# Kernel tuning notes

Measured on AMD Instinct MI355X. Metric: run time of the kernel, lower is better.

Reference implementation:

```python
import jax, jax.numpy as jnp
import numpy as np

N_NODES = 50000
N_EDGES = 800000
D_IN = 96
HID = 128


def _glorot(key, shape):
    fan_in, fan_out = shape[0], shape[1]
    lim = np.sqrt(6.0 / (fan_in + fan_out)).astype(np.float32)
    return jax.random.uniform(key, shape, jnp.float32, -lim, lim)


def setup_inputs() -> dict:
    key = jax.random.key(0)
    ks = jax.random.split(key, 12)
    x = jax.random.normal(ks[0], (N_NODES, D_IN), jnp.float32)
    edge_index = jax.random.randint(ks[1], (2, N_EDGES), 0, N_NODES)
    return {
        "x": x,
        "edge_index": edge_index,
        "W_in": _glorot(ks[2], (D_IN, HID)),
        "b_in": jnp.zeros((HID,), jnp.float32),
        "W1": _glorot(ks[3], (HID, HID)),
        "b1": jnp.zeros((HID,), jnp.float32),
        "W2": _glorot(ks[4], (HID, HID)),
        "b2": jnp.zeros((HID,), jnp.float32),
        "Wm1": _glorot(ks[5], (2 * HID, HID)),
        "bm1": jnp.zeros((HID,), jnp.float32),
        "Wm2": _glorot(ks[6], (HID, 1)),
        "bm2": jnp.zeros((1,), jnp.float32),
    }


def _gcn_conv(h, W, b, src, dst, n_nodes):
    # PyG GCNConv with add_self_loops=True, normalize=True:
    # out = D^{-1/2} (A + I) D^{-1/2} (h W) + b, aggregating x_j (source) into dst.
    loop = jnp.arange(n_nodes)
    row = jnp.concatenate([src, loop])  # source / j
    col = jnp.concatenate([dst, loop])  # target / i
    deg = jax.ops.segment_sum(jnp.ones(row.shape, h.dtype), col, num_segments=n_nodes)
    dinv = jnp.where(deg > 0, jax.lax.rsqrt(deg), 0.0)
    norm = dinv[row] * dinv[col]  # [E+N]
    xw = h @ W  # [N, H]
    msg = xw[row] * norm[:, None]  # gather + scale, [E+N, H]
    out = jax.ops.segment_sum(msg, col, num_segments=n_nodes)  # scatter-add
    return out + b


def reference(x, edge_index, W_in, b_in, W1, b1, W2, b2, Wm1, bm1, Wm2, bm2):
    src, dst = edge_index[0], edge_index[1]
    n = x.shape[0]
    h = jax.nn.relu(x @ W_in + b_in)  # dropout is identity at inference
    h = jax.nn.relu(_gcn_conv(h, W1, b1, src, dst, n))
    h = jax.nn.relu(_gcn_conv(h, W2, b2, src, dst, n))
    ef = jnp.concatenate([h[src], h[dst]], axis=1)  # [E, 2H]
    hid = jax.nn.relu(ef @ Wm1 + bm1)
    logits = (hid @ Wm2 + bm2)[:, 0]  # [E]
    return logits
```

## Files before the change

### kernel.cpp

```cpp
#include <hip/hip_runtime.h>

#define N_NODES 50000
#define N_EDGES 800000
#define D_IN 96
#define HID 128
#define NB 391
#define BCAP 3072
#define AECAP 1408

typedef __attribute__((ext_vector_type(8))) _Float16 halfx8;
typedef __attribute__((ext_vector_type(4))) _Float16 half4v;
typedef __attribute__((ext_vector_type(2))) _Float16 half2v;
typedef __attribute__((ext_vector_type(16))) float f32x16;
typedef __attribute__((ext_vector_type(8))) float f32x8;

__device__ inline float dot2acc(half2v a, half2v b, float c) {
#if __has_builtin(__builtin_amdgcn_fdot2)
    return __builtin_amdgcn_fdot2(a, b, c, false);
#else
    return c + (float)a[0] * (float)b[0] + (float)a[1] * (float)b[1];
#endif
}

__device__ inline halfx8 relu8(halfx8 s) {
#if __has_builtin(__builtin_elementwise_max)
    return __builtin_elementwise_max(s, (halfx8)0);
#else
    halfx8 r;
#pragma unroll
    for (int i = 0; i < 8; i++) r[i] = s[i] > (_Float16)0 ? s[i] : (_Float16)0;
    return r;
#endif
}

__global__ __launch_bounds__(256) void hist_pack_kernel(const int* __restrict__ dst,
                                                        int* __restrict__ bhist,
                                                        const float* __restrict__ W_in,
                                                        const float* __restrict__ W1,
                                                        const float* __restrict__ W2,
                                                        const float* __restrict__ Wm1,
                                                        const float* __restrict__ Wm2,
                                                        _Float16* __restrict__ packed) {
    __shared__ int lh[NB];
    int t = threadIdx.x;
    if (blockIdx.x < 196) {
        for (int i = t; i < NB; i += 256) lh[i] = 0;
        __syncthreads();
        int base = blockIdx.x * 4096;
#pragma unroll
        for (int i = 0; i < 16; i++) {
            int e = base + i * 256 + t;
            if (e < N_EDGES) atomicAdd(&lh[dst[e] >> 7], 1);
        }
        __syncthreads();
        for (int i = t; i < NB; i += 256) atomicAdd(&bhist[i], lh[i]);
        return;
    }
    int g = (blockIdx.x - 196) * 256 + t;
    if (g >= 77952) return;
    if (g >= 77824) { packed[g] = (_Float16)Wm2[g - 77824]; return; }
    const float* Wsrc;
    int K, u;
    if (g < 12288)      { Wsrc = W_in;            K = 96;  u = g; }
    else if (g < 28672) { Wsrc = W1;              K = 128; u = g - 12288; }
    else if (g < 45056) { Wsrc = W2;              K = 128; u = g - 28672; }
    else if (g < 61440) { Wsrc = Wm1;             K = 128; u = g - 45056; }
    else                { Wsrc = Wm1 + 128 * 128; K = 128; u = g - 61440; }
    int steps = K >> 4;
    int cb = u / (steps * 512);
    int rem = u - cb * steps * 512;
    int s = rem >> 9;
    int lane = (rem >> 3) & 63;
    int j = rem & 7;
    int k = s * 16 + ((lane >> 5) << 3) + j;
    int n = (cb << 5) + (lane & 31);
    packed[g] = (_Float16)Wsrc[k * 128 + n];
}

__global__ __launch_bounds__(512) void scan_buckets_kernel(const int* __restrict__ bhist,
                                                           int* __restrict__ boff,
                                                           int* __restrict__ bcursor) {
    __shared__ int s[512];
    int t = threadIdx.x;
    int v = (t < NB) ? bhist[t] : 0;
    s[t] = v;
    __syncthreads();
    for (int off = 1; off < 512; off <<= 1) {
        int u = (t >= off) ? s[t - off] : 0;
        __syncthreads();
        s[t] += u;
        __syncthreads();
    }
    if (t < NB) {
        int ex = s[t] - v;
        boff[t] = ex;
        bcursor[t] = ex;
    }
    if (t == NB - 1) boff[NB] = s[t];
}

__global__ __launch_bounds__(512) void bin_kernel(const int* __restrict__ src,
                                                  const int* __restrict__ dst,
                                                  int* __restrict__ bcursor,
                                                  unsigned long long* __restrict__ binned) {
    __shared__ int lh[NB];
    __shared__ int gbs[NB];
    int t = threadIdx.x;
    for (int i = t; i < NB; i += 512) lh[i] = 0;
    __syncthreads();
    int base = blockIdx.x * 8192;
    unsigned long long pk[16];
    int bb[16], rk[16];
#pragma unroll
    for (int i = 0; i < 16; i++) {
        int e = base + i * 512 + t;
        bb[i] = -1;
        if (e < N_EDGES) {
            int s = src[e], d = dst[e];
            int b = d >> 7;
            bb[i] = b;
            pk[i] = ((unsigned long long)s << 27) |
                    ((unsigned long long)(d & 127) << 20) | (unsigned long long)e;
            rk[i] = atomicAdd(&lh[b], 1);
        }
    }
    __syncthreads();
    for (int i = t; i < NB; i += 512) gbs[i] = atomicAdd(&bcursor[i], lh[i]);
    __syncthreads();
#pragma unroll
    for (int i = 0; i < 16; i++) {
        if (bb[i] >= 0) binned[gbs[bb[i]] + rk[i]] = pk[i];
    }
}

__global__ __launch_bounds__(256) void bucket_sort_kernel(const unsigned long long* __restrict__ binned,
                                                          const int* __restrict__ boff,
                                                          int* __restrict__ ce_src,
                                                          int* __restrict__ ce_eid,
                                                          int* __restrict__ ce_dst,
                                                          int* __restrict__ csr_ptr,
                                                          float* __restrict__ dinv) {
    __shared__ int2 sorted[BCAP];
    __shared__ int cntA[128], sc[128];
    int b = blockIdx.x;
    int t = threadIdx.x;
    int base = boff[b];
    int k = boff[b + 1] - base;
    if (k > BCAP) k = BCAP;
    if (t < 128) cntA[t] = 0;
    __syncthreads();
    unsigned long long pk[12];
    int rk[12];
#pragma unroll
    for (int m = 0; m < 12; m++) {
        int i = t + m * 256;
        rk[m] = -1;
        if (i < k) {
            unsigned long long p = binned[base + i];
            pk[m] = p;
            int d = (int)((p >> 20) & 127);
            rk[m] = atomicAdd(&cntA[d], 1);
        }
    }
    __syncthreads();
    if (t < 128) sc[t] = cntA[t];
    __syncthreads();
    for (int off = 1; off < 128; off <<= 1) {
        int u = 0;
        if (t < 128 && t >= off) u = sc[t - off];
        __syncthreads();
        if (t < 128) sc[t] += u;
        __syncthreads();
    }
#pragma unroll
    for (int m = 0; m < 12; m++) {
        if (rk[m] >= 0) {
            unsigned long long p = pk[m];
            int d = (int)((p >> 20) & 127);
            int pos = sc[d] - cntA[d] + rk[m];
            int srcn = (int)(p >> 27);
            int eid = (int)(p & 0xFFFFF);
            sorted[pos] = make_int2(srcn | (d << 16), eid);
        }
    }
    __syncthreads();
    for (int i = t; i < k; i += 256) {
        int2 se = sorted[i];
        ce_src[base + i] = se.x & 0xFFFF;
        ce_eid[base + i] = se.y;
        ce_dst[base + i] = (b << 7) + (se.x >> 16);
    }
    if (t < 128) {
        int node = (b << 7) + t;
        if (node < N_NODES) {
            csr_ptr[node] = base + sc[t] - cntA[t];
            dinv[node] = 1.0f / sqrtf((float)(cntA[t] + 1));
        }
    }
    if (b == NB - 1 && t == 0) csr_ptr[N_NODES] = boff[NB];
}

__global__ __launch_bounds__(256) void fused_in_kernel(const float* __restrict__ x,
                                                       const _Float16* __restrict__ WpIn,
                                                       const _Float16* __restrict__ Wp1,
                                                       const float* __restrict__ b_in,
                                                       const float* __restrict__ dinv,
                                                       _Float16* __restrict__ y1, int M) {
    __shared__ _Float16 As[32 * 104];
    __shared__ _Float16 Hs[32 * 136];
    int tid = threadIdx.x;
    int M0 = blockIdx.x * 32;
    for (int i = tid; i < 32 * 24; i += 256) {
        int r = i / 24, c = i - r * 24;
        float4 v = make_float4(0.f, 0.f, 0.f, 0.f);
        int row = M0 + r;
        if (row < M) v = *(const float4*)&x[(size_t)row * 96 + c * 4];
        half2v a = {(_Float16)v.x, (_Float16)v.y};
        half2v b = {(_Float16)v.z, (_Float16)v.w};
        *(half2v*)&As[r * 104 + c * 4] = a;
        *(half2v*)&As[r * 104 + c * 4 + 2] = b;
    }
    __syncthreads();

    int wave = tid >> 6, lane = tid & 63;
    int col = wave * 32 + (lane & 31);
    {
        const halfx8* bp = (const halfx8*)WpIn + (size_t)wave * 6 * 64 + lane;
        const _Float16* arow = &As[(lane & 31) * 104 + ((lane >> 5) << 3)];
        f32x16 acc = {};
#pragma unroll
        for (int s = 0; s < 6; s++) {
            halfx8 a = *(const halfx8*)&arow[s * 16];
            acc = __builtin_amdgcn_mfma_f32_32x32x16_f16(a, bp[s * 64], acc, 0, 0, 0);
        }
        float bA = b_in[col];
#pragma unroll
        for (int r = 0; r < 16; r++) {
            int rl = (r & 3) + 8 * (r >> 2) + 4 * (lane >> 5);
            Hs[rl * 136 + col] = (_Float16)fmaxf(acc[r] + bA, 0.f);
        }
    }
    __syncthreads();
    {
        const halfx8* bp = (const halfx8*)Wp1 + (size_t)wave * 8 * 64 + lane;
        const _Float16* arow = &Hs[(lane & 31) * 136 + ((lane >> 5) << 3)];
        f32x16 acc = {};
#pragma unroll
        for (int s = 0; s < 8; s++) {
            halfx8 a = *(const halfx8*)&arow[s * 16];
            acc = __builtin_amdgcn_mfma_f32_32x32x16_f16(a, bp[s * 64], acc, 0, 0, 0);
        }
#pragma unroll
        for (int r = 0; r < 16; r++) {
            int rl = (r & 3) + 8 * (r >> 2) + 4 * (lane >> 5);
            int grow = M0 + rl;
            if (grow < M) {
                y1[((size_t)wave * N_NODES + grow) * 32 + (lane & 31)] =
                    (_Float16)(acc[r] * dinv[grow]);
            }
        }
    }
}

__global__ __launch_bounds__(256) void gemm_f16_kernel(const _Float16* __restrict__ A,
                                                       const _Float16* __restrict__ Wp,
                                                       const float* __restrict__ bias,
                                                       const float* __restrict__ rowscale,
                                                       _Float16* __restrict__ out,
                                                       int M, int steps, int dorelu) {
    const int K = 128;
    __shared__ _Float16 As[32 * 136];
    int tid = threadIdx.x;
    int M0 = blockIdx.x * 32;
    int stride = K + 8;
    for (int i = tid; i < 32 * 16; i += 256) {
        int r = i >> 4, c = i & 15;
        uint4 v = make_uint4(0, 0, 0, 0);
        int row = M0 + r;
        if (row < M)
            v = *(const uint4*)&A[((size_t)(c >> 2) * N_NODES + row) * 32 + (c & 3) * 8];
        *(uint4*)&As[r * stride + c * 8] = v;
    }
    __syncthreads();

    int wave = tid >> 6, lane = tid & 63;
    const halfx8* bp = (const halfx8*)Wp + (size_t)wave * steps * 64 + lane;
    const _Float16* arow = &As[(lane & 31) * stride + ((lane >> 5) << 3)];
    f32x16 acc = {};
    for (int s = 0; s < steps; s++) {
        halfx8 a = *(const halfx8*)&arow[s * 16];
        acc = __builtin_amdgcn_mfma_f32_32x32x16_f16(a, bp[s * 64], acc, 0, 0, 0);
    }
    int col = wave * 32 + (lane & 31);
    float bA = bias ? bias[col] : 0.f;
#pragma unroll
    for (int r = 0; r < 16; r++) {
        int rl = (r & 3) + 8 * (r >> 2) + 4 * (lane >> 5);
        int grow = M0 + rl;
        if (grow < M) {
            float sc = rowscale ? rowscale[grow] : 1.f;
            float v0 = (acc[r] + bA) * sc;
            if (dorelu) v0 = fmaxf(v0, 0.f);
            out[((size_t)wave * N_NODES + grow) * 32 + (lane & 31)] = (_Float16)v0;
        }
    }
}

__global__ __launch_bounds__(256) void gemm_uv_kernel(const _Float16* __restrict__ A,
                                                      const _Float16* __restrict__ WpU,
                                                      const _Float16* __restrict__ WpV,
                                                      const float* __restrict__ bm1,
                                                      _Float16* __restrict__ U,
                                                      _Float16* __restrict__ V,
                                                      int M) {
    const int K = 128, steps = 8;
    __shared__ _Float16 As[32 * 136];
    int tid = threadIdx.x;
    int M0 = blockIdx.x * 32;
    int stride = K + 8;
    for (int i = tid; i < 32 * 16; i += 256) {
        int r = i >> 4, c = i & 15;
        uint4 v = make_uint4(0, 0, 0, 0);
        int row = M0 + r;
        if (row < M)
            v = *(const uint4*)&A[((size_t)(c >> 2) * N_NODES + row) * 32 + (c & 3) * 8];
        *(uint4*)&As[r * stride + c * 8] = v;
    }
    __syncthreads();

    int wave = tid >> 6, lane = tid & 63;
    const halfx8* bu = (const halfx8*)WpU + (size_t)wave * steps * 64 + lane;
    const halfx8* bv = (const halfx8*)WpV + (size_t)wave * steps * 64 + lane;
    const _Float16* arow = &As[(lane & 31) * stride + ((lane >> 5) << 3)];
    f32x16 au = {}, av = {};
#pragma unroll
    for (int s = 0; s < steps; s++) {
        halfx8 a = *(const halfx8*)&arow[s * 16];
        au = __builtin_amdgcn_mfma_f32_32x32x16_f16(a, bu[s * 64], au, 0, 0, 0);
        av = __builtin_amdgcn_mfma_f32_32x32x16_f16(a, bv[s * 64], av, 0, 0, 0);
    }
    int col = wave * 32 + (lane & 31);
    float bA = bm1[col];
#pragma unroll
    for (int r = 0; r < 16; r++) {
        int rl = (r & 3) + 8 * (r >> 2) + 4 * (lane >> 5);
        int grow = M0 + rl;
        if (grow < M) {
            U[(size_t)grow * 128 + col] = (_Float16)(au[r] + bA);
            V[(size_t)grow * 128 + col] = (_Float16)av[r];
        }
    }
}

__global__ __launch_bounds__(256, 6) void aggregate_kernel(const _Float16* __restrict__ y,
                                                           const float* __restrict__ dinv,
                                                           const int* __restrict__ ptr,
                                                           const int* __restrict__ ce_src,
                                                           const float* __restrict__ bias,
                                                           _Float16* __restrict__ out) {
    __shared__ int sidx[AECAP];
    __shared__ int sptr[65];
    int b = blockIdx.x;
    int sl = (b & 7) >> 1;
    int o = ((b >> 3) << 1) + (b & 1);
    int node0 = o * 64;
    int tid = threadIdx.x;
    if (tid < 65) {
        int nn = node0 + tid;
        sptr[tid] = ptr[nn < N_NODES ? nn : N_NODES];
    }
    __syncthreads();
    int base = sptr[0];
    int tot = sptr[64] - base;
    bool fit = (tot <= AECAP);
    if (fit) {
        for (int i = tid; i < tot; i += 256) sidx[i] = ce_src[base + i] << 6;
    }
    __syncthreads();

    int g = tid >> 2;
    int l = tid & 3;
    int nodeIdx = node0 + g;
    int node = nodeIdx < N_NODES ? nodeIdx : N_NODES - 1;
    float di = dinv[node];
    const char* ysl = (const char*)y + (size_t)sl * (N_NODES * 64) + (size_t)l * 16;
    halfx8 self = *(const halfx8*)(ysl + (size_t)node * 64);
    f32x8 acc = __builtin_convertvector(self, f32x8);
    int s0 = sptr[g], s1 = sptr[g + 1];

    if (fit) {
        int j = s0 - base, e = s1 - base;
        for (; j + 7 < e; j += 8) {
            halfx8 v0 = *(const halfx8*)(ysl + sidx[j]);
            halfx8 v1 = *(const halfx8*)(ysl + sidx[j + 1]);
            halfx8 v2 = *(const halfx8*)(ysl + sidx[j + 2]);
            halfx8 v3 = *(const halfx8*)(ysl + sidx[j + 3]);
            halfx8 v4 = *(const halfx8*)(ysl + sidx[j + 4]);
            halfx8 v5 = *(const halfx8*)(ysl + sidx[j + 5]);
            halfx8 v6 = *(const halfx8*)(ysl + sidx[j + 6]);
            halfx8 v7 = *(const halfx8*)(ysl + sidx[j + 7]);
            __builtin_amdgcn_sched_barrier(0);
            acc += __builtin_convertvector(v0, f32x8);
            acc += __builtin_convertvector(v1, f32x8);
            acc += __builtin_convertvector(v2, f32x8);
            acc += __builtin_convertvector(v3, f32x8);
            acc += __builtin_convertvector(v4, f32x8);
            acc += __builtin_convertvector(v5, f32x8);
            acc += __builtin_convertvector(v6, f32x8);
            acc += __builtin_convertvector(v7, f32x8);
        }
        for (; j + 3 < e; j += 4) {
            halfx8 v0 = *(const halfx8*)(ysl + sidx[j]);
            halfx8 v1 = *(const halfx8*)(ysl + sidx[j + 1]);
            halfx8 v2 = *(const halfx8*)(ysl + sidx[j + 2]);
            halfx8 v3 = *(const halfx8*)(ysl + sidx[j + 3]);
            __builtin_amdgcn_sched_barrier(0);
            acc += __builtin_convertvector(v0, f32x8);
            acc += __builtin_convertvector(v1, f32x8);
            acc += __builtin_convertvector(v2, f32x8);
            acc += __builtin_convertvector(v3, f32x8);
        }
        for (; j < e; j++) {
            halfx8 v = *(const halfx8*)(ysl + sidx[j]);
            acc += __builtin_convertvector(v, f32x8);
        }
    } else {
        for (int j = s0; j < s1; j++) {
            halfx8 v = *(const halfx8*)(ysl + ((size_t)ce_src[j] << 6));
            acc += __builtin_convertvector(v, f32x8);
        }
    }
    if (nodeIdx < N_NODES) {
        const float* bp = &bias[sl * 32 + l * 8];
        halfx8 ov;
#pragma unroll
        for (int k = 0; k < 8; k++) {
            ov[k] = (_Float16)fmaxf(di * acc[k] + bp[k], 0.f);
        }
        *(halfx8*)&out[((size_t)sl * N_NODES + nodeIdx) * 32 + l * 8] = ov;
    }
}

__global__ __launch_bounds__(256) void edge_mlp_kernel(const _Float16* __restrict__ Ub,
                                                       const _Float16* __restrict__ Vb,
                                                       const int* __restrict__ ce_src,
                                                       const int* __restrict__ ce_eid,
                                                       const int* __restrict__ ce_dst,
                                                       const _Float16* __restrict__ Wm2h,
                                                       const float* __restrict__ bm2,
                                                       float* __restrict__ out) {
    __shared__ int ssrc[128], sdst[128], seid[128];
    int tid = threadIdx.x;
    int e0 = blockIdx.x * 128;
    if (tid < 128) {
        ssrc[tid] = ce_src[e0 + tid];
        seid[tid] = ce_eid[e0 + tid];
    } else {
        sdst[tid - 128] = ce_dst[e0 + tid - 128];
    }
    __syncthreads();
    int g = tid >> 4;
    int l = tid & 15;
    halfx8 wv = *(const halfx8*)&Wm2h[l * 8];
    half2v w0 = {wv[0], wv[1]}, w1 = {wv[2], wv[3]}, w2 = {wv[4], wv[5]}, w3 = {wv[6], wv[7]};
    halfx8 uu[8], vv[8];
#pragma unroll
    for (int k = 0; k < 8; k++) {
        int e = g + 16 * k;
        uu[k] = *(const halfx8*)&Ub[(size_t)ssrc[e] * 128 + l * 8];
        vv[k] = *(const halfx8*)&Vb[(size_t)sdst[e] * 128 + l * 8];
    }
    __builtin_amdgcn_sched_barrier(0);
    float p[8];
#pragma unroll
    for (int k = 0; k < 8; k++) {
        halfx8 s = relu8(uu[k] + vv[k]);
        half2v s0 = {s[0], s[1]}, s1 = {s[2], s[3]}, s2 = {s[4], s[5]}, s3 = {s[6], s[7]};
        float acc = dot2acc(s0, w0, 0.f);
        acc = dot2acc(s1, w1, acc);
        acc = dot2acc(s2, w2, acc);
        p[k] = dot2acc(s3, w3, acc);
    }
#pragma unroll
    for (int d = 1; d < 16; d <<= 1) {
#pragma unroll
        for (int k = 0; k < 8; k++) p[k] += __shfl_xor(p[k], d);
    }
    if (l == 0) {
        float bb = bm2[0];
#pragma unroll
        for (int k = 0; k < 8; k++) out[seid[g + 16 * k]] = p[k] + bb;
    }
}

extern "C" void kernel_launch(void* const* d_in, const int* in_sizes, int n_in,
                              void* d_out, int out_size, void* d_ws, size_t ws_size,
                              hipStream_t stream) {
    const float* x    = (const float*)d_in[0];
    const int* eidx   = (const int*)d_in[1];
    const float* W_in = (const float*)d_in[2];
    const float* b_in = (const float*)d_in[3];
    const float* W1   = (const float*)d_in[4];
    const float* b1   = (const float*)d_in[5];
    const float* W2   = (const float*)d_in[6];
    const float* b2   = (const float*)d_in[7];
    const float* Wm1  = (const float*)d_in[8];
    const float* bm1  = (const float*)d_in[9];
    const float* Wm2  = (const float*)d_in[10];
    const float* bm2  = (const float*)d_in[11];
    float* out = (float*)d_out;
    const int* src = eidx;
    const int* dst = eidx + N_EDGES;

    char* w = (char*)d_ws;
    size_t off = 0;
    auto alloc = [&](size_t bytes) -> char* {
        char* p = w + off;
        off = (off + bytes + 255) & ~(size_t)255;
        return p;
    };
    int* bhist    = (int*)alloc((size_t)NB * 4);
    int* boff     = (int*)alloc((size_t)(NB + 1) * 4);
    int* bcursor  = (int*)alloc((size_t)NB * 4);
    int* csr_ptr  = (int*)alloc((size_t)(N_NODES + 1) * 4);
    float* dinv   = (float*)alloc((size_t)N_NODES * 4);
    unsigned long long* binned = (unsigned long long*)alloc((size_t)N_EDGES * 8);
    int* ce_src   = (int*)alloc((size_t)N_EDGES * 4);
    int* ce_eid   = (int*)alloc((size_t)N_EDGES * 4);
    int* ce_dst   = (int*)alloc((size_t)N_EDGES * 4);
    _Float16* Wp  = (_Float16*)alloc((size_t)77952 * 2);
    _Float16* y1  = (_Float16*)alloc((size_t)N_NODES * HID * 2);
    _Float16* y2  = (_Float16*)alloc((size_t)N_NODES * HID * 2);
    _Float16* hbuf = (_Float16*)alloc((size_t)N_NODES * HID * 2);
    _Float16* Ub  = (_Float16*)alloc((size_t)N_NODES * HID * 2);
    _Float16* Vb  = (_Float16*)alloc((size_t)N_NODES * HID * 2);

    const _Float16* WpIn  = Wp;
    const _Float16* Wp1   = Wp + 12288;
    const _Float16* Wp2   = Wp + 28672;
    const _Float16* WpM1a = Wp + 45056;
    const _Float16* WpM1b = Wp + 61440;
    const _Float16* Wm2h  = Wp + 77824;

    hipMemsetAsync(bhist, 0, (size_t)NB * 4, stream);
    hist_pack_kernel<<<196 + 305, 256, 0, stream>>>(dst, bhist, W_in, W1, W2, Wm1, Wm2, Wp);
    scan_buckets_kernel<<<1, 512, 0, stream>>>(bhist, boff, bcursor);
    bin_kernel<<<98, 512, 0, stream>>>(src, dst, bcursor, binned);
    bucket_sort_kernel<<<NB, 256, 0, stream>>>(binned, boff, ce_src, ce_eid, ce_dst,
                                               csr_ptr, dinv);

    int gblocks = (N_NODES + 31) / 32;
    int ablocks = 782 * 4;
    fused_in_kernel<<<gblocks, 256, 0, stream>>>(x, WpIn, Wp1, b_in, dinv, y1, N_NODES);
    aggregate_kernel<<<ablocks, 256, 0, stream>>>(y1, dinv, csr_ptr, ce_src, b1, hbuf);
    gemm_f16_kernel<<<gblocks, 256, 0, stream>>>(hbuf, Wp2, nullptr, dinv, y2,
                                                 N_NODES, 8, 0);
    aggregate_kernel<<<ablocks, 256, 0, stream>>>(y2, dinv, csr_ptr, ce_src, b2, hbuf);
    gemm_uv_kernel<<<gblocks, 256, 0, stream>>>(hbuf, WpM1a, WpM1b, bm1, Ub, Vb, N_NODES);
    edge_mlp_kernel<<<N_EDGES / 128, 256, 0, stream>>>(Ub, Vb, ce_src, ce_eid, ce_dst,
                                                       Wm2h, bm2, out);
}
```

Baseline: 238.5 us.

## Restructure edge MLP to iterate CSR per destination node, reusing V row

The edge MLP kernel now assigns 64 destination nodes per block and walks each node's CSR edge range, loading the node's V row once into registers and gathering only U rows per edge. This removes the ce_dst array, so the sort kernel no longer writes it and the edge kernel no longer reads it, and it halves the gathered feature traffic for the destination side. In exchange, work per 16-lane group now depends on node degree, which risks load imbalance and partial 4-edge unroll tails. Edge indices are staged in LDS, with a fallback global path when a block's edge count exceeds the LDS capacity.

```diff
diff --git a/kernel.cpp b/kernel.cpp
--- a/kernel.cpp
+++ b/kernel.cpp
@@ -137,7 +137,6 @@
                                                           const int* __restrict__ boff,
                                                           int* __restrict__ ce_src,
                                                           int* __restrict__ ce_eid,
-                                                          int* __restrict__ ce_dst,
                                                           int* __restrict__ csr_ptr,
                                                           float* __restrict__ dinv) {
     __shared__ int2 sorted[BCAP];
@@ -180,15 +179,14 @@
             int pos = sc[d] - cntA[d] + rk[m];
             int srcn = (int)(p >> 27);
             int eid = (int)(p & 0xFFFFF);
-            sorted[pos] = make_int2(srcn | (d << 16), eid);
+            sorted[pos] = make_int2(srcn, eid);
         }
     }
     __syncthreads();
     for (int i = t; i < k; i += 256) {
         int2 se = sorted[i];
-        ce_src[base + i] = se.x & 0xFFFF;
+        ce_src[base + i] = se.x;
         ce_eid[base + i] = se.y;
-        ce_dst[base + i] = (b << 7) + (se.x >> 16);
     }
     if (t < 128) {
         int node = (b << 7) + t;
@@ -441,55 +439,113 @@
     }
 }
 
-__global__ __launch_bounds__(256) void edge_mlp_kernel(const _Float16* __restrict__ Ub,
-                                                       const _Float16* __restrict__ Vb,
-                                                       const int* __restrict__ ce_src,
-                                                       const int* __restrict__ ce_eid,
-                                                       const int* __restrict__ ce_dst,
-                                                       const _Float16* __restrict__ Wm2h,
-                                                       const float* __restrict__ bm2,
-                                                       float* __restrict__ out) {
-    __shared__ int ssrc[128], sdst[128], seid[128];
+__global__ __launch_bounds__(256, 6) void edge_mlp_kernel(const _Float16* __restrict__ Ub,
+                                                          const _Float16* __restrict__ Vb,
+                                                          const int* __restrict__ ptr,
+                                                          const int* __restrict__ ce_src,
+                                                          const int* __restrict__ ce_eid,
+                                                          const _Float16* __restrict__ Wm2h,
+                                                          const float* __restrict__ bm2,
+                                                          float* __restrict__ out) {
+    __shared__ int sidx[AECAP];
+    __shared__ int seid[AECAP];
+    __shared__ int sptr[65];
+    int node0 = blockIdx.x * 64;
     int tid = threadIdx.x;
-    int e0 = blockIdx.x * 128;
-    if (tid < 128) {
-        ssrc[tid] = ce_src[e0 + tid];
-        seid[tid] = ce_eid[e0 + tid];
-    } else {
-        sdst[tid - 128] = ce_dst[e0 + tid - 128];
-    }
-    __syncthreads();
+    if (tid < 65) {
+        int nn = node0 + tid;
+        sptr[tid] = ptr[nn < N_NODES ? nn : N_NODES];
+    }
+    __syncthreads();
+    int base = sptr[0];
+    int tot = sptr[64] - base;
+    bool fit = (tot <= AECAP);
+    if (fit) {
+        for (int i = tid; i < tot; i += 256) {
+            sidx[i] = ce_src[base + i] << 8;
+            seid[i] = ce_eid[base + i];
+        }
+    }
+    __syncthreads();
+
     int g = tid >> 4;
     int l = tid & 15;
     halfx8 wv = *(const halfx8*)&Wm2h[l * 8];
     half2v w0 = {wv[0], wv[1]}, w1 = {wv[2], wv[3]}, w2 = {wv[4], wv[5]}, w3 = {wv[6], wv[7]};
-    halfx8 uu[8], vv[8];
-#pragma unroll
-    for (int k = 0; k < 8; k++) {
-        int e = g + 16 * k;
-        uu[k] = *(const halfx8*)&Ub[(size_t)ssrc[e] * 128 + l * 8];
-        vv[k] = *(const halfx8*)&Vb[(size_t)sdst[e] * 128 + l * 8];
-    }
-    __builtin_amdgcn_sched_barrier(0);
-    float p[8];
-#pragma unroll
-    for (int k = 0; k < 8; k++) {
-        halfx8 s = relu8(uu[k] + vv[k]);
-        half2v s0 = {s[0], s[1]}, s1 = {s[2], s[3]}, s2 = {s[4], s[5]}, s3 = {s[6], s[7]};
-        float acc = dot2acc(s0, w0, 0.f);
-        acc = dot2acc(s1, w1, acc);
-        acc = dot2acc(s2, w2, acc);
-        p[k] = dot2acc(s3, w3, acc);
-    }
-#pragma unroll
-    for (int d = 1; d < 16; d <<= 1) {
-#pragma unroll
-        for (int k = 0; k < 8; k++) p[k] += __shfl_xor(p[k], d);
-    }
-    if (l == 0) {
-        float bb = bm2[0];
-#pragma unroll
-        for (int k = 0; k < 8; k++) out[seid[g + 16 * k]] = p[k] + bb;
+    float bb = bm2[0];
+    const char* Uc = (const char*)Ub + (size_t)l * 16;
+
+#pragma unroll
+    for (int ns = 0; ns < 4; ns++) {
+        int nl = ns * 16 + g;
+        int nodeIdx = node0 + nl;
+        int node = nodeIdx < N_NODES ? nodeIdx : N_NODES - 1;
+        halfx8 vreg = *(const halfx8*)&Vb[(size_t)node * 128 + l * 8];
+        int s0 = sptr[nl], s1 = sptr[nl + 1];
+
+        if (fit) {
+            int j = s0 - base, e = s1 - base;
+            for (; j + 3 < e; j += 4) {
+                halfx8 u0 = *(const halfx8*)(Uc + sidx[j]);
+                halfx8 u1 = *(const halfx8*)(Uc + sidx[j + 1]);
+                halfx8 u2 = *(const halfx8*)(Uc + sidx[j + 2]);
+                halfx8 u3 = *(const halfx8*)(Uc + sidx[j + 3]);
+                __builtin_amdgcn_sched_barrier(0);
+                float p0, p1, p2, p3;
+                {
+                    halfx8 s = relu8(u0 + vreg);
+                    half2v s0v = {s[0], s[1]}, s1v = {s[2], s[3]}, s2v = {s[4], s[5]}, s3v = {s[6], s[7]};
+                    p0 = dot2acc(s3v, w3, dot2acc(s2v, w2, dot2acc(s1v, w1, dot2acc(s0v, w0, 0.f))));
+                }
+                {
+                    halfx8 s = relu8(u1 + vreg);
+                    half2v s0v = {s[0], s[1]}, s1v = {s[2], s[3]}, s2v = {s[4], s[5]}, s3v = {s[6], s[7]};
+                    p1 = dot2acc(s3v, w3, dot2acc(s2v, w2, dot2acc(s1v, w1, dot2acc(s0v, w0, 0.f))));
+                }
+                {
+                    halfx8 s = relu8(u2 + vreg);
+                    half2v s0v = {s[0], s[1]}, s1v = {s[2], s[3]}, s2v = {s[4], s[5]}, s3v = {s[6], s[7]};
+                    p2 = dot2acc(s3v, w3, dot2acc(s2v, w2, dot2acc(s1v, w1, dot2acc(s0v, w0, 0.f))));
+                }
+                {
+                    halfx8 s = relu8(u3 + vreg);
+                    half2v s0v = {s[0], s[1]}, s1v = {s[2], s[3]}, s2v = {s[4], s[5]}, s3v = {s[6], s[7]};
+                    p3 = dot2acc(s3v, w3, dot2acc(s2v, w2, dot2acc(s1v, w1, dot2acc(s0v, w0, 0.f))));
+                }
+#pragma unroll
+                for (int d = 1; d < 16; d <<= 1) {
+                    p0 += __shfl_xor(p0, d);
+                    p1 += __shfl_xor(p1, d);
+                    p2 += __shfl_xor(p2, d);
+                    p3 += __shfl_xor(p3, d);
+                }
+                if (l == 0) {
+                    out[seid[j]]     = p0 + bb;
+                    out[seid[j + 1]] = p1 + bb;
+                    out[seid[j + 2]] = p2 + bb;
+                    out[seid[j + 3]] = p3 + bb;
+                }
+            }
+            for (; j < e; j++) {
+                halfx8 u = *(const halfx8*)(Uc + sidx[j]);
+                halfx8 s = relu8(u + vreg);
+                half2v s0v = {s[0], s[1]}, s1v = {s[2], s[3]}, s2v = {s[4], s[5]}, s3v = {s[6], s[7]};
+                float p = dot2acc(s3v, w3, dot2acc(s2v, w2, dot2acc(s1v, w1, dot2acc(s0v, w0, 0.f))));
+#pragma unroll
+                for (int d = 1; d < 16; d <<= 1) p += __shfl_xor(p, d);
+                if (l == 0) out[seid[j]] = p + bb;
+            }
+        } else {
+            for (int j = s0; j < s1; j++) {
+                halfx8 u = *(const halfx8*)(Uc + ((size_t)ce_src[j] << 8));
+                halfx8 s = relu8(u + vreg);
+                half2v s0v = {s[0], s[1]}, s1v = {s[2], s[3]}, s2v = {s[4], s[5]}, s3v = {s[6], s[7]};
+                float p = dot2acc(s3v, w3, dot2acc(s2v, w2, dot2acc(s1v, w1, dot2acc(s0v, w0, 0.f))));
+#pragma unroll
+                for (int d = 1; d < 16; d <<= 1) p += __shfl_xor(p, d);
+                if (l == 0) out[ce_eid[j]] = p + bb;
+            }
+        }
     }
 }
 
@@ -527,7 +583,6 @@
     unsigned long long* binned = (unsigned long long*)alloc((size_t)N_EDGES * 8);
     int* ce_src   = (int*)alloc((size_t)N_EDGES * 4);
     int* ce_eid   = (int*)alloc((size_t)N_EDGES * 4);
-    int* ce_dst   = (int*)alloc((size_t)N_EDGES * 4);
     _Float16* Wp  = (_Float16*)alloc((size_t)77952 * 2);
     _Float16* y1  = (_Float16*)alloc((size_t)N_NODES * HID * 2);
     _Float16* y2  = (_Float16*)alloc((size_t)N_NODES * HID * 2);
@@ -546,17 +601,18 @@
     hist_pack_kernel<<<196 + 305, 256, 0, stream>>>(dst, bhist, W_in, W1, W2, Wm1, Wm2, Wp);
     scan_buckets_kernel<<<1, 512, 0, stream>>>(bhist, boff, bcursor);
     bin_kernel<<<98, 512, 0, stream>>>(src, dst, bcursor, binned);
-    bucket_sort_kernel<<<NB, 256, 0, stream>>>(binned, boff, ce_src, ce_eid, ce_dst,
+    bucket_sort_kernel<<<NB, 256, 0, stream>>>(binned, boff, ce_src, ce_eid,
                                                csr_ptr, dinv);
 
     int gblocks = (N_NODES + 31) / 32;
     int ablocks = 782 * 4;
+    int eblocks = (N_NODES + 63) / 64;
     fused_in_kernel<<<gblocks, 256, 0, stream>>>(x, WpIn, Wp1, b_in, dinv, y1, N_NODES);
     aggregate_kernel<<<ablocks, 256, 0, stream>>>(y1, dinv, csr_ptr, ce_src, b1, hbuf);
     gemm_f16_kernel<<<gblocks, 256, 0, stream>>>(hbuf, Wp2, nullptr, dinv, y2,
                                                  N_NODES, 8, 0);
     aggregate_kernel<<<ablocks, 256, 0, stream>>>(y2, dinv, csr_ptr, ce_src, b2, hbuf);
     gemm_uv_kernel<<<gblocks, 256, 0, stream>>>(hbuf, WpM1a, WpM1b, bm1, Ub, Vb, N_NODES);
-    edge_mlp_kernel<<<N_EDGES / 128, 256, 0, stream>>>(Ub, Vb, ce_src, ce_eid, ce_dst,
-                                                       Wm2h, bm2, out);
-}
+    edge_mlp_kernel<<<eblocks, 256, 0, stream>>>(Ub, Vb, csr_ptr, ce_src, ce_eid,
+                                                 Wm2h, bm2, out);
+}
```

Measured after the change: 243.0 us. About the same (+1.9%).

## Replace bucketed two-pass edge sort with per-node atomic counting sort

Applied to the files above, without the earlier changes.

The bucket histogram, bin and in-shared-memory bucket sort are replaced by a per-node degree histogram built with global atomics, a two-level block scan over nodes, and a scatter that claims slots with per-node atomic cursors. Source and destination are packed into one 32-bit word, which drops the separate ce_dst array and cuts index traffic in the aggregate and edge-MLP kernels. The cost is contended global atomics and scattered, poorly coalesced writes in the scatter step. Edge order within each node is no longer deterministic, so floating-point summation order can vary between runs.

```diff
diff --git a/kernel.cpp b/kernel.cpp
--- a/kernel.cpp
+++ b/kernel.cpp
@@ -4,12 +4,9 @@
 #define N_EDGES 800000
 #define D_IN 96
 #define HID 128
-#define NB 391
-#define BCAP 3072
 #define AECAP 1408
 
 typedef __attribute__((ext_vector_type(8))) _Float16 halfx8;
-typedef __attribute__((ext_vector_type(4))) _Float16 half4v;
 typedef __attribute__((ext_vector_type(2))) _Float16 half2v;
 typedef __attribute__((ext_vector_type(16))) float f32x16;
 typedef __attribute__((ext_vector_type(8))) float f32x8;
@@ -34,26 +31,21 @@
 }
 
 __global__ __launch_bounds__(256) void hist_pack_kernel(const int* __restrict__ dst,
-                                                        int* __restrict__ bhist,
+                                                        int* __restrict__ nodeCnt,
                                                         const float* __restrict__ W_in,
                                                         const float* __restrict__ W1,
                                                         const float* __restrict__ W2,
                                                         const float* __restrict__ Wm1,
                                                         const float* __restrict__ Wm2,
                                                         _Float16* __restrict__ packed) {
-    __shared__ int lh[NB];
     int t = threadIdx.x;
     if (blockIdx.x < 196) {
-        for (int i = t; i < NB; i += 256) lh[i] = 0;
-        __syncthreads();
         int base = blockIdx.x * 4096;
 #pragma unroll
         for (int i = 0; i < 16; i++) {
             int e = base + i * 256 + t;
-            if (e < N_EDGES) atomicAdd(&lh[dst[e] >> 7], 1);
-        }
-        __syncthreads();
-        for (int i = t; i < NB; i += 256) atomicAdd(&bhist[i], lh[i]);
+            if (e < N_EDGES) atomicAdd(&nodeCnt[dst[e]], 1);
+        }
         return;
     }
     int g = (blockIdx.x - 196) * 256 + t;
@@ -77,127 +69,68 @@
     packed[g] = (_Float16)Wsrc[k * 128 + n];
 }
 
-__global__ __launch_bounds__(512) void scan_buckets_kernel(const int* __restrict__ bhist,
-                                                           int* __restrict__ boff,
-                                                           int* __restrict__ bcursor) {
-    __shared__ int s[512];
+__global__ __launch_bounds__(256) void scan_node_kernel(const int* __restrict__ nodeCnt,
+                                                        int* __restrict__ csr_loc,
+                                                        int* __restrict__ bsum,
+                                                        float* __restrict__ dinv) {
+    __shared__ int s[256];
     int t = threadIdx.x;
-    int v = (t < NB) ? bhist[t] : 0;
-    s[t] = v;
-    __syncthreads();
-    for (int off = 1; off < 512; off <<= 1) {
+    int n = blockIdx.x * 256 + t;
+    int cnt = (n < N_NODES) ? nodeCnt[n] : 0;
+    s[t] = cnt;
+    __syncthreads();
+    for (int off = 1; off < 256; off <<= 1) {
         int u = (t >= off) ? s[t - off] : 0;
         __syncthreads();
         s[t] += u;
         __syncthreads();
     }
-    if (t < NB) {
-        int ex = s[t] - v;
-        boff[t] = ex;
-        bcursor[t] = ex;
-    }
-    if (t == NB - 1) boff[NB] = s[t];
-}
-
-__global__ __launch_bounds__(512) void bin_kernel(const int* __restrict__ src,
-                                                  const int* __restrict__ dst,
-                                                  int* __restrict__ bcursor,
-                                                  unsigned long long* __restrict__ binned) {
-    __shared__ int lh[NB];
-    __shared__ int gbs[NB];
+    if (n < N_NODES) {
+        csr_loc[n] = s[t] - cnt;
+        dinv[n] = 1.0f / sqrtf((float)(cnt + 1));
+    }
+    if (t == 255) bsum[blockIdx.x] = s[t];
+}
+
+__global__ __launch_bounds__(256) void scan_finalize_kernel(const int* __restrict__ csr_loc,
+                                                            const int* __restrict__ bsum,
+                                                            int* __restrict__ csr_ptr,
+                                                            int* __restrict__ cursor) {
+    __shared__ int lh[256];
     int t = threadIdx.x;
-    for (int i = t; i < NB; i += 512) lh[i] = 0;
-    __syncthreads();
-    int base = blockIdx.x * 8192;
-    unsigned long long pk[16];
-    int bb[16], rk[16];
+    int b = blockIdx.x;
+    lh[t] = (t < b && t < 196) ? bsum[t] : 0;
+    __syncthreads();
+    for (int off = 128; off >= 1; off >>= 1) {
+        if (t < off) lh[t] += lh[t + off];
+        __syncthreads();
+    }
+    int offset = lh[0];
+    int n = b * 256 + t;
+    if (n < N_NODES) {
+        int val = csr_loc[n] + offset;
+        csr_ptr[n] = val;
+        cursor[n] = val;
+    }
+    if (b == 0 && t == 0) csr_ptr[N_NODES] = N_EDGES;
+}
+
+__global__ __launch_bounds__(256) void scatter_kernel(const int* __restrict__ src,
+                                                      const int* __restrict__ dst,
+                                                      int* __restrict__ cursor,
+                                                      unsigned int* __restrict__ ce_sd,
+                                                      int* __restrict__ ce_eid) {
+    int base = blockIdx.x * 4096;
 #pragma unroll
     for (int i = 0; i < 16; i++) {
-        int e = base + i * 512 + t;
-        bb[i] = -1;
+        int e = base + i * 256 + threadIdx.x;
         if (e < N_EDGES) {
-            int s = src[e], d = dst[e];
-            int b = d >> 7;
-            bb[i] = b;
-            pk[i] = ((unsigned long long)s << 27) |
-                    ((unsigned long long)(d & 127) << 20) | (unsigned long long)e;
-            rk[i] = atomicAdd(&lh[b], 1);
-        }
-    }
-    __syncthreads();
-    for (int i = t; i < NB; i += 512) gbs[i] = atomicAdd(&bcursor[i], lh[i]);
-    __syncthreads();
-#pragma unroll
-    for (int i = 0; i < 16; i++) {
-        if (bb[i] >= 0) binned[gbs[bb[i]] + rk[i]] = pk[i];
-    }
-}
-
-__global__ __launch_bounds__(256) void bucket_sort_kernel(const unsigned long long* __restrict__ binned,
-                                                          const int* __restrict__ boff,
-                                                          int* __restrict__ ce_src,
-                                                          int* __restrict__ ce_eid,
-                                                          int* __restrict__ ce_dst,
-                                                          int* __restrict__ csr_ptr,
-                                                          float* __restrict__ dinv) {
-    __shared__ int2 sorted[BCAP];
-    __shared__ int cntA[128], sc[128];
-    int b = blockIdx.x;
-    int t = threadIdx.x;
-    int base = boff[b];
-    int k = boff[b + 1] - base;
-    if (k > BCAP) k = BCAP;
-    if (t < 128) cntA[t] = 0;
-    __syncthreads();
-    unsigned long long pk[12];
-    int rk[12];
-#pragma unroll
-    for (int m = 0; m < 12; m++) {
-        int i = t + m * 256;
-        rk[m] = -1;
-        if (i < k) {
-            unsigned long long p = binned[base + i];
-            pk[m] = p;
-            int d = (int)((p >> 20) & 127);
-            rk[m] = atomicAdd(&cntA[d], 1);
-        }
-    }
-    __syncthreads();
-    if (t < 128) sc[t] = cntA[t];
-    __syncthreads();
-    for (int off = 1; off < 128; off <<= 1) {
-        int u = 0;
-        if (t < 128 && t >= off) u = sc[t - off];
-        __syncthreads();
-        if (t < 128) sc[t] += u;
-        __syncthreads();
-    }
-#pragma unroll
-    for (int m = 0; m < 12; m++) {
-        if (rk[m] >= 0) {
-            unsigned long long p = pk[m];
-            int d = (int)((p >> 20) & 127);
-            int pos = sc[d] - cntA[d] + rk[m];
-            int srcn = (int)(p >> 27);
-            int eid = (int)(p & 0xFFFFF);
-            sorted[pos] = make_int2(srcn | (d << 16), eid);
-        }
-    }
-    __syncthreads();
-    for (int i = t; i < k; i += 256) {
-        int2 se = sorted[i];
-        ce_src[base + i] = se.x & 0xFFFF;
-        ce_eid[base + i] = se.y;
-        ce_dst[base + i] = (b << 7) + (se.x >> 16);
-    }
-    if (t < 128) {
-        int node = (b << 7) + t;
-        if (node < N_NODES) {
-            csr_ptr[node] = base + sc[t] - cntA[t];
-            dinv[node] = 1.0f / sqrtf((float)(cntA[t] + 1));
-        }
-    }
-    if (b == NB - 1 && t == 0) csr_ptr[N_NODES] = boff[NB];
+            unsigned int s = (unsigned int)src[e], d = (unsigned int)dst[e];
+            int pos = atomicAdd(&cursor[d], 1);
+            ce_sd[pos] = s | (d << 16);
+            ce_eid[pos] = e;
+        }
+    }
 }
 
 __global__ __launch_bounds__(256) void fused_in_kernel(const float* __restrict__ x,
@@ -355,7 +288,7 @@
 __global__ __launch_bounds__(256, 6) void aggregate_kernel(const _Float16* __restrict__ y,
                                                            const float* __restrict__ dinv,
                                                            const int* __restrict__ ptr,
-                                                           const int* __restrict__ ce_src,
+                                                           const unsigned int* __restrict__ ce_sd,
                                                            const float* __restrict__ bias,
                                                            _Float16* __restrict__ out) {
     __shared__ int sidx[AECAP];
@@ -374,7 +307,8 @@
     int tot = sptr[64] - base;
     bool fit = (tot <= AECAP);
     if (fit) {
-        for (int i = tid; i < tot; i += 256) sidx[i] = ce_src[base + i] << 6;
+        for (int i = tid; i < tot; i += 256)
+            sidx[i] = (int)((ce_sd[base + i] & 0xFFFFu) << 6);
     }
     __syncthreads();
 
@@ -426,7 +360,7 @@
         }
     } else {
         for (int j = s0; j < s1; j++) {
-            halfx8 v = *(const halfx8*)(ysl + ((size_t)ce_src[j] << 6));
+            halfx8 v = *(const halfx8*)(ysl + ((size_t)(ce_sd[j] & 0xFFFFu) << 6));
             acc += __builtin_convertvector(v, f32x8);
         }
     }
@@ -443,20 +377,19 @@
 
 __global__ __launch_bounds__(256) void edge_mlp_kernel(const _Float16* __restrict__ Ub,
                                                        const _Float16* __restrict__ Vb,
-                                                       const int* __restrict__ ce_src,
+                                                       const unsigned int* __restrict__ ce_sd,
                                                        const int* __restrict__ ce_eid,
-                                                       const int* __restrict__ ce_dst,
                                                        const _Float16* __restrict__ Wm2h,
                                                        const float* __restrict__ bm2,
                                                        float* __restrict__ out) {
-    __shared__ int ssrc[128], sdst[128], seid[128];
+    __shared__ unsigned int ssd[128];
+    __shared__ int seid[128];
     int tid = threadIdx.x;
     int e0 = blockIdx.x * 128;
     if (tid < 128) {
-        ssrc[tid] = ce_src[e0 + tid];
-        seid[tid] = ce_eid[e0 + tid];
+        ssd[tid] = ce_sd[e0 + tid];
     } else {
-        sdst[tid - 128] = ce_dst[e0 + tid - 128];
+        seid[tid - 128] = ce_eid[e0 + tid - 128];
     }
     __syncthreads();
     int g = tid >> 4;
@@ -466,9 +399,9 @@
     halfx8 uu[8], vv[8];
 #pragma unroll
     for (int k = 0; k < 8; k++) {
-        int e = g + 16 * k;
-        uu[k] = *(const halfx8*)&Ub[(size_t)ssrc[e] * 128 + l * 8];
-        vv[k] = *(const halfx8*)&Vb[(size_t)sdst[e] * 128 + l * 8];
+        unsigned int sd = ssd[g + 16 * k];
+        uu[k] = *(const halfx8*)&Ub[(size_t)(sd & 0xFFFFu) * 128 + l * 8];
+        vv[k] = *(const halfx8*)&Vb[(size_t)(sd >> 16) * 128 + l * 8];
     }
     __builtin_amdgcn_sched_barrier(0);
     float p[8];
@@ -519,15 +452,14 @@
         off = (off + bytes + 255) & ~(size_t)255;
         return p;
     };
-    int* bhist    = (int*)alloc((size_t)NB * 4);
-    int* boff     = (int*)alloc((size_t)(NB + 1) * 4);
-    int* bcursor  = (int*)alloc((size_t)NB * 4);
+    int* nodeCnt  = (int*)alloc((size_t)N_NODES * 4);
+    int* csr_loc  = (int*)alloc((size_t)N_NODES * 4);
+    int* bsum     = (int*)alloc((size_t)196 * 4);
     int* csr_ptr  = (int*)alloc((size_t)(N_NODES + 1) * 4);
+    int* cursor   = (int*)alloc((size_t)N_NODES * 4);
     float* dinv   = (float*)alloc((size_t)N_NODES * 4);
-    unsigned long long* binned = (unsigned long long*)alloc((size_t)N_EDGES * 8);
-    int* ce_src   = (int*)alloc((size_t)N_EDGES * 4);
+    unsigned int* ce_sd = (unsigned int*)alloc((size_t)N_EDGES * 4);
     int* ce_eid   = (int*)alloc((size_t)N_EDGES * 4);
-    int* ce_dst   = (int*)alloc((size_t)N_EDGES * 4);
     _Float16* Wp  = (_Float16*)alloc((size_t)77952 * 2);
     _Float16* y1  = (_Float16*)alloc((size_t)N_NODES * HID * 2);
     _Float16* y2  = (_Float16*)alloc((size_t)N_NODES * HID * 2);
@@ -542,21 +474,20 @@
     const _Float16* WpM1b = Wp + 61440;
     const _Float16* Wm2h  = Wp + 77824;
 
-    hipMemsetAsync(bhist, 0, (size_t)NB * 4, stream);
-    hist_pack_kernel<<<196 + 305, 256, 0, stream>>>(dst, bhist, W_in, W1, W2, Wm1, Wm2, Wp);
-    scan_buckets_kernel<<<1, 512, 0, stream>>>(bhist, boff, bcursor);
-    bin_kernel<<<98, 512, 0, stream>>>(src, dst, bcursor, binned);
-    bucket_sort_kernel<<<NB, 256, 0, stream>>>(binned, boff, ce_src, ce_eid, ce_dst,
-                                               csr_ptr, dinv);
+    hipMemsetAsync(nodeCnt, 0, (size_t)N_NODES * 4, stream);
+    hist_pack_kernel<<<196 + 305, 256, 0, stream>>>(dst, nodeCnt, W_in, W1, W2, Wm1, Wm2, Wp);
+    scan_node_kernel<<<196, 256, 0, stream>>>(nodeCnt, csr_loc, bsum, dinv);
+    scan_finalize_kernel<<<196, 256, 0, stream>>>(csr_loc, bsum, csr_ptr, cursor);
+    scatter_kernel<<<196, 256, 0, stream>>>(src, dst, cursor, ce_sd, ce_eid);
 
     int gblocks = (N_NODES + 31) / 32;
     int ablocks = 782 * 4;
     fused_in_kernel<<<gblocks, 256, 0, stream>>>(x, WpIn, Wp1, b_in, dinv, y1, N_NODES);
-    aggregate_kernel<<<ablocks, 256, 0, stream>>>(y1, dinv, csr_ptr, ce_src, b1, hbuf);
+    aggregate_kernel<<<ablocks, 256, 0, stream>>>(y1, dinv, csr_ptr, ce_sd, b1, hbuf);
     gemm_f16_kernel<<<gblocks, 256, 0, stream>>>(hbuf, Wp2, nullptr, dinv, y2,
                                                  N_NODES, 8, 0);
-    aggregate_kernel<<<ablocks, 256, 0, stream>>>(y2, dinv, csr_ptr, ce_src, b2, hbuf);
+    aggregate_kernel<<<ablocks, 256, 0, stream>>>(y2, dinv, csr_ptr, ce_sd, b2, hbuf);
     gemm_uv_kernel<<<gblocks, 256, 0, stream>>>(hbuf, WpM1a, WpM1b, bm1, Ub, Vb, N_NODES);
-    edge_mlp_kernel<<<N_EDGES / 128, 256, 0, stream>>>(Ub, Vb, ce_src, ce_eid, ce_dst,
+    edge_mlp_kernel<<<N_EDGES / 128, 256, 0, stream>>>(Ub, Vb, ce_sd, ce_eid,
                                                        Wm2h, bm2, out);
 }
```

Result: slower. 292.2 us (+22.5%).
